# Kernel optimization log

Hardware: AMD Instinct MI355X
Metric: run time of the kernel (lower is better)

The kernel has to match this reference:

```python
import jax, jax.numpy as jnp
import numpy as np

B, C, H, W = 64, 96, 56, 56
KS = 7
HIDDEN = 512
EPS = 1e-5


def setup_inputs() -> dict:
    key = jax.random.key(0)
    k1, k2, k3 = jax.random.split(key, 3)
    hw = H * W
    return {
        "x": jax.random.normal(k1, (B, C, H, W), dtype=jnp.float32),
        "ln_gamma": jnp.ones((hw,), jnp.float32),
        "ln_beta": jnp.zeros((hw,), jnp.float32),
        "w0": jax.random.normal(k2, (hw, HIDDEN), jnp.float32) * 0.02,
        "b0": jnp.zeros((HIDDEN,), jnp.float32),
        "w1": jax.random.normal(k3, (HIDDEN, KS * KS), jnp.float32) * 0.02,
        "b1": jnp.zeros((KS * KS,), jnp.float32),
        "attn_bias": jnp.zeros((B * C,), jnp.float32),
    }


def reference(x, ln_gamma, ln_beta, w0, b0, w1, b1, attn_bias):
    b, c, h, w = x.shape
    a = x.reshape(b, c, h * w)  # B C (HW)
    # LayerNorm over flattened spatial dim
    mu = jnp.mean(a, axis=-1, keepdims=True)
    var = jnp.mean(jnp.square(a - mu), axis=-1, keepdims=True)
    a = (a - mu) * jax.lax.rsqrt(var + EPS) * ln_gamma + ln_beta
    # 2-layer MLP -> per-(B,C) KxK kernel; exact GELU matches torch nn.GELU()
    a = jax.nn.gelu(jnp.einsum("bcn,nd->bcd", a, w0) + b0, approximate=False)
    a = jnp.einsum("bcd,dk->bck", a, w1) + b1  # (B, C, K*K)
    weight = a.reshape(b * c, 1, KS, KS)  # OIHW, one input channel per group
    xin = x.reshape(1, b * c, h, w)
    pad = KS // 2
    out = jax.lax.conv_general_dilated(
        xin, weight,
        window_strides=(1, 1),
        padding=[(pad, pad), (pad, pad)],
        dimension_numbers=("NCHW", "OIHW", "NCHW"),
        feature_group_count=b * c,
    )
    out = out + attn_bias.reshape(1, b * c, 1, 1)
    return out.reshape(b, c, h, w)
```

## Files before the change

kernel.cpp:

```cpp
#include <hip/hip_runtime.h>
#include <hip/hip_bf16.h>

#define BB 64
#define CC 96
#define HH 56
#define WW 56
#define HWS 3136
#define BC 6144
#define HIDDEN 512
#define KS 7
#define KK2 49
#define K1 3136
#define N1 512
#define EPS 1e-5f

typedef __attribute__((ext_vector_type(8))) short short8;
typedef __attribute__((ext_vector_type(4))) float f32x4;

static __device__ __forceinline__ unsigned short f2bf(float f) {
    union { float f; unsigned int u; } un; un.f = f;
    unsigned int r = un.u + 0x7fffu + ((un.u >> 16) & 1u);
    return (unsigned short)(r >> 16);
}

__global__ __launch_bounds__(256) void ln_kernel(const float* __restrict__ x,
                                                 const float* __restrict__ gamma,
                                                 const float* __restrict__ beta,
                                                 unsigned short* __restrict__ a) {
    const int row = blockIdx.x;
    const float4* xr = (const float4*)(x + (size_t)row * HWS);
    float sum = 0.f, sq = 0.f;
    for (int i = threadIdx.x; i < HWS / 4; i += 256) {
        float4 v = xr[i];
        sum += (v.x + v.y) + (v.z + v.w);
        sq = fmaf(v.x, v.x, sq); sq = fmaf(v.y, v.y, sq);
        sq = fmaf(v.z, v.z, sq); sq = fmaf(v.w, v.w, sq);
    }
    #pragma unroll
    for (int off = 32; off > 0; off >>= 1) {
        sum += __shfl_down(sum, off, 64);
        sq  += __shfl_down(sq,  off, 64);
    }
    __shared__ float s1[4], s2[4];
    const int lane = threadIdx.x & 63, wave = threadIdx.x >> 6;
    if (lane == 0) { s1[wave] = sum; s2[wave] = sq; }
    __syncthreads();
    sum = s1[0] + s1[1] + s1[2] + s1[3];
    sq  = s2[0] + s2[1] + s2[2] + s2[3];
    const float mu = sum * (1.f / HWS);
    const float var = fmaf(-mu, mu, sq * (1.f / HWS));
    const float rs = rsqrtf(var + EPS);
    const float4* gr = (const float4*)gamma;
    const float4* br = (const float4*)beta;
    ushort4* ar = (ushort4*)(a + (size_t)row * HWS);
    for (int i = threadIdx.x; i < HWS / 4; i += 256) {
        float4 v = xr[i], g = gr[i], b = br[i];
        ushort4 o;
        o.x = f2bf((v.x - mu) * rs * g.x + b.x);
        o.y = f2bf((v.y - mu) * rs * g.y + b.y);
        o.z = f2bf((v.z - mu) * rs * g.z + b.z);
        o.w = f2bf((v.w - mu) * rs * g.w + b.w);
        ar[i] = o;
    }
}

__global__ __launch_bounds__(256) void w0t_kernel(const float* __restrict__ w0,
                                                  unsigned short* __restrict__ w0t) {
    __shared__ float tile[64][65];
    const int kb = blockIdx.x * 64;
    const int nb = blockIdx.y * 64;
    for (int i = threadIdx.x; i < 64 * 64; i += 256) {
        int r = i >> 6, c = i & 63;
        tile[r][c] = w0[(size_t)(kb + r) * N1 + nb + c];
    }
    __syncthreads();
    for (int i = threadIdx.x; i < 64 * 64; i += 256) {
        int r = i >> 6, c = i & 63;
        w0t[(size_t)(nb + r) * K1 + kb + c] = f2bf(tile[c][r]);
    }
}

__global__ __launch_bounds__(256) void gemm1_kernel(const unsigned short* __restrict__ A,
                                                    const unsigned short* __restrict__ Bt,
                                                    const float* __restrict__ b0,
                                                    float* __restrict__ hidden) {
    __shared__ __align__(16) char smem[32768];
    const int t = threadIdx.x;
    const int wave = t >> 6, lane = t & 63;
    const int wm = wave >> 1, wn = wave & 1;
    const int tm = blockIdx.x * 64;
    const int tn = blockIdx.y * 64;

    f32x4 acc[2][2] = {};

    auto stage = [&](int buf, int k0) {
        #pragma unroll
        for (int it = 0; it < 2; ++it) {
            int chunk = it * 256 + t;
            int row = chunk >> 3;
            int cb = (chunk & 7) << 4;
            int sb = cb ^ ((row & 7) << 4);
            const char* gA = (const char*)(A + (size_t)(tm + row) * K1 + k0) + sb;
            const char* gB = (const char*)(Bt + (size_t)(tn + row) * K1 + k0) + sb;
            char* ldsA = smem + buf * 16384 + it * 4096 + wave * 1024;
            char* ldsB = smem + buf * 16384 + 8192 + it * 4096 + wave * 1024;
            __builtin_amdgcn_global_load_lds(
                (const __attribute__((address_space(1))) unsigned int*)gA,
                (__attribute__((address_space(3))) unsigned int*)ldsA, 16, 0, 0);
            __builtin_amdgcn_global_load_lds(
                (const __attribute__((address_space(1))) unsigned int*)gB,
                (__attribute__((address_space(3))) unsigned int*)ldsB, 16, 0, 0);
        }
    };

    auto compute = [&](int buf) {
        const char* base = smem + buf * 16384;
        #pragma unroll
        for (int kk = 0; kk < 2; ++kk) {
            short8 af[2], bfr[2];
            const int kbase = kk * 64 + ((lane >> 4) << 4);
            #pragma unroll
            for (int i = 0; i < 2; ++i) {
                int row = wm * 32 + i * 16 + (lane & 15);
                af[i] = *(const short8*)(base + row * 128 + (kbase ^ ((row & 7) << 4)));
            }
            #pragma unroll
            for (int j = 0; j < 2; ++j) {
                int row = wn * 32 + j * 16 + (lane & 15);
                bfr[j] = *(const short8*)(base + 8192 + row * 128 + (kbase ^ ((row & 7) << 4)));
            }
            #pragma unroll
            for (int i = 0; i < 2; ++i)
                #pragma unroll
                for (int j = 0; j < 2; ++j)
                    acc[i][j] = __builtin_amdgcn_mfma_f32_16x16x32_bf16(af[i], bfr[j], acc[i][j], 0, 0, 0);
        }
    };

    stage(0, 0);
    __syncthreads();
    int buf = 0;
    for (int ks = 0; ks < 48; ++ks) {
        stage(buf ^ 1, (ks + 1) * 64);
        compute(buf);
        __syncthreads();
        buf ^= 1;
    }
    compute(buf);

    #pragma unroll
    for (int j = 0; j < 2; ++j) {
        const int gc = tn + wn * 32 + j * 16 + (lane & 15);
        const float bias = b0[gc];
        #pragma unroll
        for (int i = 0; i < 2; ++i) {
            #pragma unroll
            for (int r = 0; r < 4; ++r) {
                int gr = tm + wm * 32 + i * 16 + ((lane >> 4) << 2) + r;
                float v = acc[i][j][r] + bias;
                float g = 0.5f * v * (1.0f + erff(v * 0.70710678118f));
                hidden[(size_t)gr * N1 + gc] = g;
            }
        }
    }
}

__global__ __launch_bounds__(256) void gemm2_kernel(const float* __restrict__ hidden,
                                                    const float* __restrict__ w1,
                                                    const float* __restrict__ b1,
                                                    float* __restrict__ kw) {
    __shared__ float hs[4][HIDDEN];
    const int row0 = blockIdx.x * 4;
    for (int i = threadIdx.x; i < (4 * HIDDEN) / 4; i += 256)
        ((float4*)hs)[i] = ((const float4*)(hidden + (size_t)row0 * HIDDEN))[i];
    __syncthreads();
    const int wrow = threadIdx.x >> 6, lane = threadIdx.x & 63;
    const int n = lane < KK2 ? lane : KK2 - 1;
    float acc = 0.f;
    #pragma unroll 8
    for (int k = 0; k < HIDDEN; ++k)
        acc = fmaf(hs[wrow][k], w1[k * KK2 + n], acc);
    if (lane < KK2)
        kw[(size_t)(row0 + wrow) * KK2 + lane] = acc + b1[lane];
}

#define TSTRIDE 68
#define TFLOATS (62 * TSTRIDE)
__global__ __launch_bounds__(256) void conv_kernel(const float* __restrict__ x,
                                                   const float* __restrict__ kw,
                                                   const float* __restrict__ attn_bias,
                                                   float* __restrict__ out) {
    __shared__ __align__(16) float tile[2][TFLOATS];
    __shared__ __align__(16) float wsm[2][52];
    const int t = threadIdx.x;
    const int plane0 = blockIdx.x * 2;
    const float* xp = x + (size_t)plane0 * HWS;

    if (t < 98) {
        int p = t / 49, j = t % 49;
        wsm[p][j] = kw[(size_t)(plane0 + p) * KK2 + j];
    }
    for (int i = t; i < 2108; i += 256) {
        int p = i / 1054;
        int rem = i - p * 1054;
        int r = rem / 17;
        int c4 = (rem - r * 17) * 4;
        const float* xpp = xp + p * HWS;
        int sr = r - 3;
        float4 v;
        float* vc = (float*)&v;
        #pragma unroll
        for (int j = 0; j < 4; ++j) {
            int sc = c4 + j - 3;
            vc[j] = (sr >= 0 && sr < HH && sc >= 0 && sc < WW) ? xpp[sr * WW + sc] : 0.f;
        }
        *(float4*)&tile[p][r * TSTRIDE + c4] = v;
    }
    __syncthreads();

    if (t < 224) {
        const int p = t / 112;
        const int idx = t - p * 112;
        const int tr = idx / 14;
        const int tc = idx - tr * 14;
        const int plane = plane0 + p;
        const int c0 = tc * 4;

        float wr[49];
        #pragma unroll
        for (int i = 0; i < 12; ++i) {
            float4 v = *(const float4*)&wsm[p][4 * i];
            wr[4 * i] = v.x; wr[4 * i + 1] = v.y; wr[4 * i + 2] = v.z; wr[4 * i + 3] = v.w;
        }
        wr[48] = wsm[p][48];

        const float bias = attn_bias[plane];
        float acc[7][4];
        #pragma unroll
        for (int o = 0; o < 7; ++o)
            #pragma unroll
            for (int j = 0; j < 4; ++j) acc[o][j] = bias;

        const float* tp = &tile[p][tr * 7 * TSTRIDE + c0];
        #pragma unroll
        for (int ir = 0; ir < 13; ++ir) {
            float rv[10];
            float4 va = *(const float4*)(tp + ir * TSTRIDE);
            float4 vb = *(const float4*)(tp + ir * TSTRIDE + 4);
            float2 vc2 = *(const float2*)(tp + ir * TSTRIDE + 8);
            rv[0] = va.x; rv[1] = va.y; rv[2] = va.z; rv[3] = va.w;
            rv[4] = vb.x; rv[5] = vb.y; rv[6] = vb.z; rv[7] = vb.w;
            rv[8] = vc2.x; rv[9] = vc2.y;
            #pragma unroll
            for (int kr = 0; kr < 7; ++kr) {
                const int o = ir - kr;
                if (o >= 0 && o < 7) {
                    #pragma unroll
                    for (int dc = 0; dc < 7; ++dc) {
                        float wv = wr[kr * 7 + dc];
                        acc[o][0] = fmaf(rv[dc],     wv, acc[o][0]);
                        acc[o][1] = fmaf(rv[dc + 1], wv, acc[o][1]);
                        acc[o][2] = fmaf(rv[dc + 2], wv, acc[o][2]);
                        acc[o][3] = fmaf(rv[dc + 3], wv, acc[o][3]);
                    }
                }
            }
        }
        float* op = out + (size_t)plane * HWS + tr * 7 * WW + c0;
        #pragma unroll
        for (int o = 0; o < 7; ++o) {
            float4 v = { acc[o][0], acc[o][1], acc[o][2], acc[o][3] };
            *(float4*)(op + o * WW) = v;
        }
    }
}

extern "C" void kernel_launch(void* const* d_in, const int* in_sizes, int n_in,
                              void* d_out, int out_size, void* d_ws, size_t ws_size,
                              hipStream_t stream) {
    const float* x        = (const float*)d_in[0];
    const float* ln_g     = (const float*)d_in[1];
    const float* ln_b     = (const float*)d_in[2];
    const float* w0       = (const float*)d_in[3];
    const float* b0       = (const float*)d_in[4];
    const float* w1       = (const float*)d_in[5];
    const float* b1       = (const float*)d_in[6];
    const float* attn_b   = (const float*)d_in[7];
    float* out = (float*)d_out;

    char* ws = (char*)d_ws;
    unsigned short* a_bf  = (unsigned short*)ws;
    unsigned short* w0t   = (unsigned short*)(ws + 38535168);
    float*          hidden = (float*)(ws + 41746432);
    float*          kw     = (float*)(ws + 54329344);

    hipLaunchKernelGGL(ln_kernel,    dim3(BC),     dim3(256), 0, stream, x, ln_g, ln_b, a_bf);
    hipLaunchKernelGGL(w0t_kernel,   dim3(49, 8),  dim3(256), 0, stream, w0, w0t);
    hipLaunchKernelGGL(gemm1_kernel, dim3(96, 8),  dim3(256), 0, stream, a_bf, w0t, b0, hidden);
    hipLaunchKernelGGL(gemm2_kernel, dim3(BC / 4), dim3(256), 0, stream, hidden, w1, b1, kw);
    hipLaunchKernelGGL(conv_kernel,  dim3(BC / 2), dim3(256), 0, stream, x, kw, attn_b, out);
}
```

Baseline: 272.4 us.

## Store hidden activations in bf16 and XOR-swizzle conv tile in shared memory

The GELU output of the first GEMM is now written as bf16, halving hidden-buffer traffic between gemm1 and gemm2. gemm2 loads bf16 rows with vector loads and uses four independent accumulators to shorten the dependency chain. The conv kernel's shared tile becomes float4 slots with an XOR swizzle on column index to reduce LDS bank conflicts, at the cost of a third full float4 read per row. Bf16 hidden values add rounding error to the generated kernel weights.

```diff
diff --git a/kernel.cpp b/kernel.cpp
--- a/kernel.cpp
+++ b/kernel.cpp
@@ -21,6 +21,10 @@
     union { float f; unsigned int u; } un; un.f = f;
     unsigned int r = un.u + 0x7fffu + ((un.u >> 16) & 1u);
     return (unsigned short)(r >> 16);
+}
+static __device__ __forceinline__ float bf2f(unsigned short u) {
+    union { unsigned int u; float f; } un; un.u = ((unsigned int)u) << 16;
+    return un.f;
 }
 
 __global__ __launch_bounds__(256) void ln_kernel(const float* __restrict__ x,
@@ -83,7 +87,7 @@
 __global__ __launch_bounds__(256) void gemm1_kernel(const unsigned short* __restrict__ A,
                                                     const unsigned short* __restrict__ Bt,
                                                     const float* __restrict__ b0,
-                                                    float* __restrict__ hidden) {
+                                                    unsigned short* __restrict__ hidden) {
     __shared__ __align__(16) char smem[32768];
     const int t = threadIdx.x;
     const int wave = t >> 6, lane = t & 63;
@@ -159,38 +163,43 @@
                 int gr = tm + wm * 32 + i * 16 + ((lane >> 4) << 2) + r;
                 float v = acc[i][j][r] + bias;
                 float g = 0.5f * v * (1.0f + erff(v * 0.70710678118f));
-                hidden[(size_t)gr * N1 + gc] = g;
+                hidden[(size_t)gr * N1 + gc] = f2bf(g);
             }
         }
     }
 }
 
-__global__ __launch_bounds__(256) void gemm2_kernel(const float* __restrict__ hidden,
+__global__ __launch_bounds__(256) void gemm2_kernel(const unsigned short* __restrict__ hidden,
                                                     const float* __restrict__ w1,
                                                     const float* __restrict__ b1,
                                                     float* __restrict__ kw) {
-    __shared__ float hs[4][HIDDEN];
+    __shared__ unsigned short hs[4][HIDDEN];
     const int row0 = blockIdx.x * 4;
-    for (int i = threadIdx.x; i < (4 * HIDDEN) / 4; i += 256)
-        ((float4*)hs)[i] = ((const float4*)(hidden + (size_t)row0 * HIDDEN))[i];
+    if (threadIdx.x < 256) {
+        ((short8*)hs)[threadIdx.x] = ((const short8*)(hidden + (size_t)row0 * HIDDEN))[threadIdx.x];
+    }
     __syncthreads();
     const int wrow = threadIdx.x >> 6, lane = threadIdx.x & 63;
     const int n = lane < KK2 ? lane : KK2 - 1;
-    float acc = 0.f;
-    #pragma unroll 8
-    for (int k = 0; k < HIDDEN; ++k)
-        acc = fmaf(hs[wrow][k], w1[k * KK2 + n], acc);
+    float a0 = 0.f, a1 = 0.f, a2 = 0.f, a3 = 0.f;
+    #pragma unroll 4
+    for (int k = 0; k < HIDDEN; k += 4) {
+        ushort4 h4 = *(const ushort4*)&hs[wrow][k];
+        a0 = fmaf(bf2f(h4.x), w1[(k    ) * KK2 + n], a0);
+        a1 = fmaf(bf2f(h4.y), w1[(k + 1) * KK2 + n], a1);
+        a2 = fmaf(bf2f(h4.z), w1[(k + 2) * KK2 + n], a2);
+        a3 = fmaf(bf2f(h4.w), w1[(k + 3) * KK2 + n], a3);
+    }
     if (lane < KK2)
-        kw[(size_t)(row0 + wrow) * KK2 + lane] = acc + b1[lane];
-}
-
-#define TSTRIDE 68
-#define TFLOATS (62 * TSTRIDE)
+        kw[(size_t)(row0 + wrow) * KK2 + lane] = (a0 + a1) + (a2 + a3) + b1[lane];
+}
+
+#define NSLOT 17
 __global__ __launch_bounds__(256) void conv_kernel(const float* __restrict__ x,
                                                    const float* __restrict__ kw,
                                                    const float* __restrict__ attn_bias,
                                                    float* __restrict__ out) {
-    __shared__ __align__(16) float tile[2][TFLOATS];
+    __shared__ __align__(16) float4 tile4[2][62 * NSLOT];
     __shared__ __align__(16) float wsm[2][52];
     const int t = threadIdx.x;
     const int plane0 = blockIdx.x * 2;
@@ -204,17 +213,18 @@
         int p = i / 1054;
         int rem = i - p * 1054;
         int r = rem / 17;
-        int c4 = (rem - r * 17) * 4;
+        int c4 = rem - r * 17;
         const float* xpp = xp + p * HWS;
         int sr = r - 3;
         float4 v;
         float* vc = (float*)&v;
         #pragma unroll
         for (int j = 0; j < 4; ++j) {
-            int sc = c4 + j - 3;
+            int sc = c4 * 4 + j - 3;
             vc[j] = (sr >= 0 && sr < HH && sc >= 0 && sc < WW) ? xpp[sr * WW + sc] : 0.f;
         }
-        *(float4*)&tile[p][r * TSTRIDE + c4] = v;
+        int sl = (c4 < 16) ? (c4 ^ (r & 7)) : 16;
+        tile4[p][r * NSLOT + sl] = v;
     }
     __syncthreads();
 
@@ -223,8 +233,8 @@
         const int idx = t - p * 112;
         const int tr = idx / 14;
         const int tc = idx - tr * 14;
+
         const int plane = plane0 + p;
-        const int c0 = tc * 4;
 
         float wr[49];
         #pragma unroll
@@ -241,16 +251,18 @@
             #pragma unroll
             for (int j = 0; j < 4; ++j) acc[o][j] = bias;
 
-        const float* tp = &tile[p][tr * 7 * TSTRIDE + c0];
         #pragma unroll
         for (int ir = 0; ir < 13; ++ir) {
+            const int rr = tr * 7 + ir;
+            const float4* rowp = &tile4[p][rr * NSLOT];
+            const int x7 = rr & 7;
+            float4 va  = rowp[tc ^ x7];
+            float4 vb  = rowp[(tc + 1) ^ x7];
+            float4 vc4 = rowp[(tc + 2) ^ x7];
             float rv[10];
-            float4 va = *(const float4*)(tp + ir * TSTRIDE);
-            float4 vb = *(const float4*)(tp + ir * TSTRIDE + 4);
-            float2 vc2 = *(const float2*)(tp + ir * TSTRIDE + 8);
             rv[0] = va.x; rv[1] = va.y; rv[2] = va.z; rv[3] = va.w;
             rv[4] = vb.x; rv[5] = vb.y; rv[6] = vb.z; rv[7] = vb.w;
-            rv[8] = vc2.x; rv[9] = vc2.y;
+            rv[8] = vc4.x; rv[9] = vc4.y;
             #pragma unroll
             for (int kr = 0; kr < 7; ++kr) {
                 const int o = ir - kr;
@@ -266,7 +278,7 @@
                 }
             }
         }
-        float* op = out + (size_t)plane * HWS + tr * 7 * WW + c0;
+        float* op = out + (size_t)plane * HWS + tr * 7 * WW + tc * 4;
         #pragma unroll
         for (int o = 0; o < 7; ++o) {
             float4 v = { acc[o][0], acc[o][1], acc[o][2], acc[o][3] };
@@ -289,10 +301,10 @@
     float* out = (float*)d_out;
 
     char* ws = (char*)d_ws;
-    unsigned short* a_bf  = (unsigned short*)ws;
-    unsigned short* w0t   = (unsigned short*)(ws + 38535168);
-    float*          hidden = (float*)(ws + 41746432);
-    float*          kw     = (float*)(ws + 54329344);
+    unsigned short* a_bf   = (unsigned short*)ws;
+    unsigned short* w0t    = (unsigned short*)(ws + 38535168);
+    unsigned short* hidden = (unsigned short*)(ws + 41746432);
+    float*          kw     = (float*)(ws + 48037888);
 
     hipLaunchKernelGGL(ln_kernel,    dim3(BC),     dim3(256), 0, stream, x, ln_g, ln_b, a_bf);
     hipLaunchKernelGGL(w0t_kernel,   dim3(49, 8),  dim3(256), 0, stream, w0, w0t);
```

Result: faster. 263.1 us (-3.4%).
